# Optimization experiments

Measured on AMD Instinct MI355X. Metric: run time of the kernel, lower is better.

Reference implementation:

```python
import jax, jax.numpy as jnp
import numpy as np

LOG_SIG_MIN, LOG_SIG_MAX = -20.0, 2.0
BN_EPS = 1e-5

def leaky_relu(x):
    return jnp.where(x >= 0, x, 0.01 * x)

def setup_inputs() -> dict:
    key = jax.random.key(0)
    ks = jax.random.split(key, 12)
    E, B, N, H, A = 8, 16384, 64, 512, 8  # encoders, batch, nagents, hidden, heads
    d = H // A
    f32 = jnp.float32
    inp = {}
    inp['states'] = jax.random.normal(ks[0], (E, B, N), dtype=f32)
    inp['pre_actions'] = jax.random.normal(ks[1], (B, H), dtype=f32)
    inp['W_enc'] = jax.random.normal(ks[2], (E, N, H), dtype=f32) / np.sqrt(N)
    inp['b_enc'] = jnp.zeros((E, H), dtype=f32)
    inp['W_pre'] = jax.random.normal(ks[3], (H, H), dtype=f32) / np.sqrt(H)
    inp['b_pre'] = jnp.zeros((H,), dtype=f32)
    inp['Wk'] = jax.random.normal(ks[4], (A, H, d), dtype=f32) / np.sqrt(H)
    inp['Wsel'] = jax.random.normal(ks[5], (A, H, d), dtype=f32) / np.sqrt(H)
    inp['Wv'] = jax.random.normal(ks[6], (A, H, d), dtype=f32) / np.sqrt(H)
    inp['bv'] = jnp.zeros((A, d), dtype=f32)
    inp['W_actor'] = jax.random.normal(ks[7], (H, H), dtype=f32) / np.sqrt(H)
    inp['b_actor'] = jnp.zeros((H,), dtype=f32)
    inp['W_mean'] = jax.random.normal(ks[8], (H, N), dtype=f32) / np.sqrt(H)
    inp['b_mean'] = jnp.zeros((N,), dtype=f32)
    inp['W_logstd'] = jax.random.normal(ks[9], (H, N), dtype=f32) / np.sqrt(H)
    inp['b_logstd'] = jnp.zeros((N,), dtype=f32)
    return inp

def reference(states, pre_actions, W_enc, b_enc, W_pre, b_pre, Wk, Wsel, Wv, bv,
              W_actor, b_actor, W_mean, b_mean, W_logstd, b_logstd):
    # states: [E, B, N]; per-encoder BatchNorm1d (training-mode batch stats, no affine)
    mu = states.mean(axis=1, keepdims=True)                      # [E,1,N]
    var = states.var(axis=1, keepdims=True)                      # biased var, as torch BN
    s_norm = (states - mu) * jax.lax.rsqrt(var + BN_EPS)
    # per-encoder Linear + LeakyReLU -> encodings [E, B, H]
    encs = leaky_relu(jnp.einsum('ebn,enh->ebh', s_norm, W_enc) + b_enc[:, None, :])
    # per-head keys/values over all encoders: [A, E, B, d]
    keys = jnp.einsum('ebh,ahd->aebd', encs, Wk)
    vals = leaky_relu(jnp.einsum('ebh,ahd->aebd', encs, Wv) + bv[:, None, None, :])
    # selector from encoded previous actions: [A, B, d]
    pre = leaky_relu(pre_actions @ W_pre + b_pre)                 # [B, H]
    sel = jnp.einsum('bh,ahd->abd', pre, Wsel)
    d = keys.shape[-1]
    logits = jnp.einsum('abd,aebd->abe', sel, keys)               # [A, B, E]
    w = jax.nn.softmax(logits / np.sqrt(d), axis=-1)
    attn = jnp.einsum('aebd,abe->abd', vals, w)                   # [A, B, d]
    B = attn.shape[1]
    actor_in = jnp.transpose(attn, (1, 0, 2)).reshape(B, -1)      # [B, A*d] head-concat
    x = jax.nn.relu(actor_in @ W_actor + b_actor)
    mean = x @ W_mean + b_mean
    log_std = jnp.clip(x @ W_logstd + b_logstd, LOG_SIG_MIN, LOG_SIG_MAX)
    return mean, log_std, actor_in
```

## Files before the change

### kernel.cpp

```cpp
#include <hip/hip_runtime.h>
#include <hip/hip_bf16.h>
#include <stdint.h>

#define E_ 8
#define B_ 16384
#define N_ 64
#define H_ 512
#define A_ 8
#define D_ 64

typedef __hip_bfloat16 bf16;
typedef __attribute__((ext_vector_type(8))) short s8v;
typedef __attribute__((ext_vector_type(4))) float f4v;

__device__ __forceinline__ float bf2f(bf16 v) { return __bfloat162float(v); }
__device__ __forceinline__ bf16 f2bf(float v) { return __float2bfloat16(v); }
__device__ __forceinline__ short f2bfs(float v) {
    bf16 b = f2bf(v); short s; __builtin_memcpy(&s, &b, 2); return s;
}
__device__ __forceinline__ float bfs2f(short s) {
    bf16 b; __builtin_memcpy(&b, &s, 2); return bf2f(b);
}

__device__ __forceinline__ void async_load16(const void* g, void* l) {
    __builtin_amdgcn_global_load_lds(
        (const __attribute__((address_space(1))) void*)g,
        (__attribute__((address_space(3))) void*)l, 16, 0, 0);
}

__device__ __forceinline__ int swz_off(int row, int krow) {
    return row * 64 + (((krow >> 3) ^ (row & 7)) << 3);
}

template <int CB>
__device__ __forceinline__ void xcd_map(int x, int nBm, int& bm, int& bn) {
    if ((nBm & 7) == 0) {
        int j = x & 7, s = x >> 3;
        bn = s & ((1 << CB) - 1);
        bm = ((s >> CB) << 3) | j;
    } else {
        bm = x >> CB;
        bn = x & ((1 << CB) - 1);
    }
}

__global__ __launch_bounds__(256) void bnPart(const float* __restrict__ states,
                                              float* __restrict__ part,
                                              bf16* __restrict__ sbf) {
    int blk = blockIdx.x;
    int e = blk >> 6, sl = blk & 63;
    int tid = threadIdx.x, n = tid & 63, rg = tid >> 6;
    const long rowBase = (long)e * B_ + (long)sl * 256;
    const float* base = states + rowBase * 64;
    float s1 = 0.f, s2 = 0.f;
    for (int i = 0; i < 64; ++i) {
        float v = base[(rg + i * 4) * 64 + n];
        s1 += v; s2 += v * v;
        sbf[(rowBase + rg + i * 4) * 64 + n] = f2bf(v);
    }
    __shared__ float sh[2][4][64];
    sh[0][rg][n] = s1; sh[1][rg][n] = s2;
    __syncthreads();
    if (tid < 64) {
        float t1 = sh[0][0][n] + sh[0][1][n] + sh[0][2][n] + sh[0][3][n];
        float t2 = sh[1][0][n] + sh[1][1][n] + sh[1][2][n] + sh[1][3][n];
        part[((long)blk * 64 + n) * 2 + 0] = t1;
        part[((long)blk * 64 + n) * 2 + 1] = t2;
    }
}

__global__ void bnFin(const float* __restrict__ part, float* __restrict__ mu_rstd) {
    int idx = blockIdx.x * blockDim.x + threadIdx.x;
    if (idx >= E_ * 64) return;
    int e = idx >> 6, n = idx & 63;
    float s1 = 0.f, s2 = 0.f;
    for (int sl = 0; sl < 64; ++sl) {
        s1 += part[(((long)e * 64 + sl) * 64 + n) * 2 + 0];
        s2 += part[(((long)e * 64 + sl) * 64 + n) * 2 + 1];
    }
    float mu = s1 / (float)B_;
    float var = s2 / (float)B_ - mu * mu;
    mu_rstd[idx * 2 + 0] = mu;
    mu_rstd[idx * 2 + 1] = rsqrtf(var + 1e-5f);
}

__global__ void foldEnc(const float* __restrict__ W_enc, const float* __restrict__ b_enc,
                        const float* __restrict__ mu_rstd,
                        bf16* __restrict__ WencfT, float* __restrict__ bencf) {
    int idx = blockIdx.x * 256 + threadIdx.x;
    int e = idx >> 9, h = idx & 511;
    float acc = b_enc[e * 512 + h];
    for (int n = 0; n < 64; ++n) {
        float mu = mu_rstd[(e * 64 + n) * 2 + 0];
        float rs = mu_rstd[(e * 64 + n) * 2 + 1];
        float w = W_enc[((long)e * 64 + n) * 512 + h];
        WencfT[((long)e * 512 + h) * 64 + n] = f2bf(w * rs);
        acc -= mu * rs * w;
    }
    bencf[e * 512 + h] = acc;
}

__global__ __launch_bounds__(256) void packAll(
    const float* __restrict__ W_pre, const float* __restrict__ W_actor,
    const float* __restrict__ Wsel, const float* __restrict__ Wk,
    const float* __restrict__ Wv, const float* __restrict__ wm,
    const float* __restrict__ wl, const float* __restrict__ pre_actions,
    bf16* __restrict__ WpreT, bf16* __restrict__ WactorT, bf16* __restrict__ WselT,
    bf16* __restrict__ WkvaT, bf16* __restrict__ WmlT, bf16* __restrict__ pa_bf) {
    int bx = blockIdx.x, tid = threadIdx.x;
    if (bx < 2048) {
        const float* in = (bx < 1024) ? W_pre : W_actor;
        bf16* out = (bx < 1024) ? WpreT : WactorT;
        int idx = (bx & 1023) * 256 + tid;
        int n = idx >> 9, k = idx & 511;
        out[idx] = f2bf(in[k * 512 + n]);
    } else if (bx < 3072) {
        int idx = (bx - 2048) * 256 + tid;
        int n = idx >> 9, h = idx & 511;
        int a = n >> 6, dd = n & 63;
        WselT[idx] = f2bf(Wsel[((long)a * 512 + h) * 64 + dd]);
    } else if (bx < 5120) {
        int idx = (bx - 3072) * 256 + tid;
        int n = idx >> 9, h = idx & 511;
        int a = n >> 7, j = n & 127;
        const float* src = (j < 64) ? Wk : Wv;
        WkvaT[idx] = f2bf(src[((long)a * 512 + h) * 64 + (j & 63)]);
    } else if (bx < 5376) {
        int idx = (bx - 5120) * 256 + tid;
        int n = idx >> 9, k = idx & 511;
        float v = (n < 64) ? wm[k * 64 + n] : wl[k * 64 + (n - 64)];
        WmlT[idx] = f2bf(v);
    } else {
        int i = (bx - 5376) * 256 + tid;
        float4 v = ((const float4*)pre_actions)[i];
        bf16 o[4] = {f2bf(v.x), f2bf(v.y), f2bf(v.z), f2bf(v.w)};
        __builtin_memcpy(pa_bf + (long)i * 4, o, 8);
    }
}

template <int ACT, int OUTF, bool HAS_BIAS, int CB>
__global__ __launch_bounds__(256) void gemm_bt(
    const bf16* __restrict__ Ag, const bf16* __restrict__ Bg,
    const float* __restrict__ bias, const float* __restrict__ bias2,
    void* __restrict__ out, void* __restrict__ out2,
    int M, int Nn, int K, long sA, long sB, long sBias, long sO) {
    const int tid = threadIdx.x, lane = tid & 63, wid = tid >> 6;
    const int wm = wid >> 1, wn = wid & 1;
    int bm, bn;
    xcd_map<CB>(blockIdx.x, gridDim.x >> CB, bm, bn);
    const int bz = blockIdx.z;
    const bf16* Aptr = Ag + (long)bz * sA + (long)bm * 128 * K;
    const bf16* Bptr = Bg + (long)bz * sB + (long)bn * 128 * K;

    __shared__ __align__(16) short sAl[128 * 64];
    __shared__ __align__(16) short sBl[128 * 64];

    const int srow = lane >> 3;
    const int scol = (((lane & 7) ^ srow) << 3);

    f4v acc[4][4];
#pragma unroll
    for (int i = 0; i < 4; ++i)
#pragma unroll
        for (int j = 0; j < 4; ++j) acc[i][j] = f4v{0.f, 0.f, 0.f, 0.f};

    for (int k0 = 0; k0 < K; k0 += 64) {
#pragma unroll
        for (int i = 0; i < 4; ++i) {
            int r = (wid * 4 + i) * 8 + srow;
            async_load16(Aptr + (long)r * K + k0 + scol, (char*)sAl + (wid * 4 + i) * 1024);
            async_load16(Bptr + (long)r * K + k0 + scol, (char*)sBl + (wid * 4 + i) * 1024);
        }
        __syncthreads();
#pragma unroll
        for (int kk = 0; kk < 64; kk += 32) {
            int krow = kk + (lane >> 4) * 8;
            s8v af[4], bfr[4];
#pragma unroll
            for (int mi = 0; mi < 4; ++mi)
                af[mi] = *(const s8v*)(sAl + swz_off(wm * 64 + mi * 16 + (lane & 15), krow));
#pragma unroll
            for (int ni = 0; ni < 4; ++ni)
                bfr[ni] = *(const s8v*)(sBl + swz_off(wn * 64 + ni * 16 + (lane & 15), krow));
#pragma unroll
            for (int mi = 0; mi < 4; ++mi)
#pragma unroll
                for (int ni = 0; ni < 4; ++ni)
                    acc[mi][ni] = __builtin_amdgcn_mfma_f32_16x16x32_bf16(
                        af[mi], bfr[ni], acc[mi][ni], 0, 0, 0);
        }
        __syncthreads();
    }

    long m0 = (long)bm * 128 + wm * 64;
    long n0 = (long)bn * 128 + wn * 64;
#pragma unroll
    for (int mi = 0; mi < 4; ++mi)
#pragma unroll
        for (int ni = 0; ni < 4; ++ni)
#pragma unroll
            for (int r = 0; r < 4; ++r) {
                long gm = m0 + mi * 16 + (lane >> 4) * 4 + r;
                long gn = n0 + ni * 16 + (lane & 15);
                float v = acc[mi][ni][r];
                if constexpr (HAS_BIAS) v += bias[sBias * bz + gn];
                if constexpr (ACT == 1) v = (v >= 0.f) ? v : 0.01f * v;
                if constexpr (ACT == 2) v = fmaxf(v, 0.f);
                if constexpr (OUTF == 0) {
                    ((bf16*)out)[(long)bz * sO + gm * Nn + gn] = f2bf(v);
                } else if constexpr (OUTF == 1) {
                    ((float*)out)[(long)bz * sO + gm * Nn + gn] = v;
                } else if constexpr (OUTF == 2) {
                    if (gn < 64) {
                        ((float*)out)[gm * 64 + gn] = v + bias[gn];
                    } else {
                        float w = v + bias2[gn - 64];
                        w = fminf(fmaxf(w, -20.f), 2.f);
                        ((float*)out2)[gm * 64 + (gn - 64)] = w;
                    }
                } else {
                    ((bf16*)out)[(gm * E_ + bz) * 512 + gn] = f2bf(v);
                }
            }
}

__global__ __launch_bounds__(256) void kv_attn(
    const bf16* __restrict__ Ag, const bf16* __restrict__ Bg,
    const float* __restrict__ bv, const float* __restrict__ sel,
    float* __restrict__ actor_f32, bf16* __restrict__ attn_bf, int b0) {
    const int tid = threadIdx.x, lane = tid & 63, wid = tid >> 6;
    const int wm = wid >> 1, wn = wid & 1;
    int bm, a;
    xcd_map<3>(blockIdx.x, gridDim.x >> 3, bm, a);
    const bf16* Aptr = Ag + (long)bm * 128 * 512;
    const bf16* Bptr = Bg + (long)a * 128 * 512;

    __shared__ __align__(16) short sA[2 * 8192];
    __shared__ __align__(16) short sB[8192];
    __shared__ float lgs[128];

    const long bgBase = (long)b0 + (long)bm * 16;

    s8v bselH[2], bselL[2];
#pragma unroll
    for (int kk = 0; kk < 2; ++kk) {
        const float* sp = sel + (bgBase + (lane & 15)) * 512 + a * 64 + kk * 32 + (lane >> 4) * 8;
#pragma unroll
        for (int j = 0; j < 8; ++j) {
            float s = sp[j] * 0.125f;
            short h = f2bfs(s);
            bselH[kk][j] = h;
            bselL[kk][j] = f2bfs(s - bfs2f(h));
        }
    }

    const int srow = lane >> 3;
    const int scol = (((lane & 7) ^ srow) << 3);

    auto stageA = [&](int kt, int buf) {
#pragma unroll
        for (int i = 0; i < 4; ++i) {
            int r = (wid * 4 + i) * 8 + srow;
            async_load16(Aptr + (long)r * 512 + kt * 64 + scol,
                         (char*)(sA + buf * 8192) + (wid * 4 + i) * 1024);
        }
    };
    auto stageB = [&](int kt) {
#pragma unroll
        for (int i = 0; i < 4; ++i) {
            int r = (wid * 4 + i) * 8 + srow;
            async_load16(Bptr + (long)r * 512 + kt * 64 + scol,
                         (char*)sB + (wid * 4 + i) * 1024);
        }
    };

    f4v acc[4][4];
#pragma unroll
    for (int i = 0; i < 4; ++i)
#pragma unroll
        for (int j = 0; j < 4; ++j) acc[i][j] = f4v{0.f, 0.f, 0.f, 0.f};

    stageA(0, 0);
    stageB(0);
    __syncthreads();
    int cur = 0;
    for (int t = 0; t < 8; ++t) {
        if (t < 7) stageA(t + 1, cur ^ 1);
        const short* sAc = sA + cur * 8192;
#pragma unroll
        for (int kk = 0; kk < 64; kk += 32) {
            int krow = kk + (lane >> 4) * 8;
            s8v af[4], bfr[4];
#pragma unroll
            for (int mi = 0; mi < 4; ++mi)
                af[mi] = *(const s8v*)(sAc + swz_off(wm * 64 + mi * 16 + (lane & 15), krow));
#pragma unroll
            for (int ni = 0; ni < 4; ++ni)
                bfr[ni] = *(const s8v*)(sB + swz_off(wn * 64 + ni * 16 + (lane & 15), krow));
#pragma unroll
            for (int mi = 0; mi < 4; ++mi)
#pragma unroll
                for (int ni = 0; ni < 4; ++ni)
                    acc[mi][ni] = __builtin_amdgcn_mfma_f32_16x16x32_bf16(
                        af[mi], bfr[ni], acc[mi][ni], 0, 0, 0);
        }
        __syncthreads();
        if (t < 7) {
            stageB(t + 1);
            __syncthreads();
        }
        cur ^= 1;
    }

    short* keysC = sA;
    short* vT    = sB;
    const int quad = lane >> 4, cl = lane & 15;
#pragma unroll
    for (int mi = 0; mi < 4; ++mi)
#pragma unroll
        for (int ni = 0; ni < 4; ++ni)
#pragma unroll
            for (int r = 0; r < 4; ++r) {
                int row = wm * 64 + mi * 16 + quad * 4 + r;
                float v = acc[mi][ni][r];
                if (wn == 0) {
                    keysC[row * 72 + ni * 16 + cl] = f2bfs(v);
                } else {
                    int d = ni * 16 + cl;
                    v += bv[a * 64 + d];
                    v = (v >= 0.f) ? v : 0.01f * v;
                    vT[d * 128 + (row ^ ((d & 15) << 3))] = f2bfs(v);
                }
            }
    __syncthreads();

    {
        f4v lgacc[2] = {f4v{0.f, 0.f, 0.f, 0.f}, f4v{0.f, 0.f, 0.f, 0.f}};
#pragma unroll
        for (int kk = 0; kk < 2; ++kk) {
#pragma unroll
            for (int mi = 0; mi < 2; ++mi) {
                s8v af = *(const s8v*)(keysC + (wid * 32 + mi * 16 + cl) * 72 +
                                       kk * 32 + quad * 8);
                lgacc[mi] = __builtin_amdgcn_mfma_f32_16x16x32_bf16(
                    af, bselH[kk], lgacc[mi], 0, 0, 0);
                lgacc[mi] = __builtin_amdgcn_mfma_f32_16x16x32_bf16(
                    af, bselL[kk], lgacc[mi], 0, 0, 0);
            }
        }
#pragma unroll
        for (int mi = 0; mi < 2; ++mi)
#pragma unroll
            for (int r = 0; r < 4; ++r) {
                int grow = wid * 32 + mi * 16 + quad * 4 + r;
                if (cl == (grow >> 3)) lgs[grow] = lgacc[mi][r];
            }
    }
    __syncthreads();

#pragma unroll
    for (int t = 0; t < 4; ++t) {
        int lb = wid * 4 + t, row0 = lb * 8;
        s8v vvv = *(const s8v*)(vT + lane * 128 + (row0 ^ ((lane & 15) << 3)));
        float lg[8], vv[8];
#pragma unroll
        for (int e = 0; e < 8; ++e) {
            vv[e] = bfs2f(vvv[e]);
            lg[e] = lgs[row0 + e];
        }
        float mx = lg[0];
#pragma unroll
        for (int e = 1; e < 8; ++e) mx = fmaxf(mx, lg[e]);
        float ssum = 0.f, w[8];
#pragma unroll
        for (int e = 0; e < 8; ++e) { w[e] = __expf(lg[e] - mx); ssum += w[e]; }
        float inv = 1.f / ssum;
        float at = 0.f;
#pragma unroll
        for (int e = 0; e < 8; ++e) at += vv[e] * (w[e] * inv);
        long o = (bgBase + lb) * 512 + a * 64 + lane;
        actor_f32[o] = at;
        attn_bf[o] = f2bf(at);
    }
}

extern "C" void kernel_launch(void* const* d_in, const int* in_sizes, int n_in,
                              void* d_out, int out_size, void* d_ws, size_t ws_size,
                              hipStream_t stream) {
    (void)in_sizes; (void)n_in; (void)out_size;
    const float* states      = (const float*)d_in[0];
    const float* pre_actions = (const float*)d_in[1];
    const float* W_enc       = (const float*)d_in[2];
    const float* b_enc       = (const float*)d_in[3];
    const float* W_pre       = (const float*)d_in[4];
    const float* b_pre       = (const float*)d_in[5];
    const float* Wk          = (const float*)d_in[6];
    const float* Wsel        = (const float*)d_in[7];
    const float* Wv          = (const float*)d_in[8];
    const float* bv          = (const float*)d_in[9];
    const float* W_actor     = (const float*)d_in[10];
    const float* b_actor     = (const float*)d_in[11];
    const float* W_mean      = (const float*)d_in[12];
    const float* b_mean      = (const float*)d_in[13];
    const float* W_logstd    = (const float*)d_in[14];
    const float* b_logstd    = (const float*)d_in[15];

    char* ws = (char*)d_ws;
    size_t off = 0;
    auto alloc = [&](size_t bytes) -> void* {
        void* p = ws + off;
        off = (off + bytes + 255) & ~(size_t)255;
        return p;
    };
    float* mu_rstd = (float*)alloc((size_t)E_ * 64 * 2 * 4);
    float* bnpart  = (float*)alloc((size_t)E_ * 64 * 64 * 2 * 4);
    bf16* WencfT   = (bf16*)alloc((size_t)E_ * 512 * 64 * 2);
    float* bencf   = (float*)alloc((size_t)E_ * 512 * 4);
    bf16* WpreT    = (bf16*)alloc((size_t)512 * 512 * 2);
    bf16* WselT    = (bf16*)alloc((size_t)512 * 512 * 2);
    bf16* WkvaT    = (bf16*)alloc((size_t)1024 * 512 * 2);
    bf16* WactorT  = (bf16*)alloc((size_t)512 * 512 * 2);
    bf16* WmlT     = (bf16*)alloc((size_t)128 * 512 * 2);
    bf16* pa_bf    = (bf16*)alloc((size_t)B_ * 512 * 2);
    bf16* p_pre    = (bf16*)alloc((size_t)B_ * 512 * 2);
    float* p_sel   = (float*)alloc((size_t)B_ * 512 * 4);
    bf16* s_bf     = (bf16*)alloc((size_t)E_ * B_ * 64 * 2);
    bf16* p_attn = pa_bf;
    bf16* p_x    = p_pre;

    size_t remaining = (ws_size > off) ? ws_size - off : 0;
    int Bc = B_;
    while (Bc > 128 && (size_t)Bc * 8192 + 4096 > remaining) Bc >>= 1;
    const int NC = B_ / Bc;
    bf16* c_encs = (bf16*)alloc((size_t)E_ * Bc * 512 * 2);

    packAll<<<13568, 256, 0, stream>>>(W_pre, W_actor, Wsel, Wk, Wv, W_mean, W_logstd,
                                       pre_actions, WpreT, WactorT, WselT, WkvaT, WmlT,
                                       pa_bf);
    bnPart<<<512, 256, 0, stream>>>(states, bnpart, s_bf);
    bnFin<<<2, 256, 0, stream>>>(bnpart, mu_rstd);
    foldEnc<<<16, 256, 0, stream>>>(W_enc, b_enc, mu_rstd, WencfT, bencf);

    gemm_bt<1, 0, true, 2><<<dim3((B_ / 128) << 2, 1, 1), 256, 0, stream>>>(
        pa_bf, WpreT, b_pre, nullptr, p_pre, nullptr, B_, 512, 512, 0, 0, 0, 0);
    gemm_bt<0, 1, false, 2><<<dim3((B_ / 128) << 2, 1, 1), 256, 0, stream>>>(
        p_pre, WselT, nullptr, nullptr, p_sel, nullptr, B_, 512, 512, 0, 0, 0, 0);

    float* actor_out = (float*)d_out + 2L * B_ * 64;
    for (int c = 0; c < NC; ++c) {
        int b0 = c * Bc;
        gemm_bt<1, 4, true, 2><<<dim3((Bc / 128) << 2, 1, E_), 256, 0, stream>>>(
            s_bf + (long)b0 * 64, WencfT, bencf, nullptr, c_encs, nullptr, Bc, 512, 64,
            (long)B_ * 64, (long)512 * 64, 512, 0);
        kv_attn<<<dim3((Bc / 16) * 8, 1, 1), 256, 0, stream>>>(
            c_encs, WkvaT, bv, p_sel, actor_out, p_attn, b0);
    }

    gemm_bt<2, 0, true, 2><<<dim3((B_ / 128) << 2, 1, 1), 256, 0, stream>>>(
        p_attn, WactorT, b_actor, nullptr, p_x, nullptr, B_, 512, 512, 0, 0, 0, 0);
    gemm_bt<0, 2, false, 0><<<dim3(B_ / 128, 1, 1), 256, 0, stream>>>(
        p_x, WmlT, b_mean, b_logstd, (float*)d_out, (float*)d_out + (long)B_ * 64,
        B_, 128, 512, 0, 0, 0, 0);
}
```

Baseline: 556.7 us.

## Process two attention heads per kv_attn block to reuse encoder tiles

Each kv_attn block now computes keys and values for two heads, using a 128x256 output tile instead of 128x128, so every staged encoder (A) tile is reused across twice as many MFMA columns and the grid is halved. Shared memory grows to 64 KB plus logits, the per-thread accumulator array doubles to 32 f4v, and the keys buffer moves to a swizzled 64-wide layout. This cuts redundant global reads of the encodings but raises register and LDS pressure, which can lower occupancy.

```diff
diff --git a/kernel.cpp b/kernel.cpp
--- a/kernel.cpp
+++ b/kernel.cpp
@@ -230,21 +230,22 @@
     float* __restrict__ actor_f32, bf16* __restrict__ attn_bf, int b0) {
     const int tid = threadIdx.x, lane = tid & 63, wid = tid >> 6;
     const int wm = wid >> 1, wn = wid & 1;
-    int bm, a;
-    xcd_map<3>(blockIdx.x, gridDim.x >> 3, bm, a);
+    int bm, hp;
+    xcd_map<2>(blockIdx.x, gridDim.x >> 2, bm, hp);
     const bf16* Aptr = Ag + (long)bm * 128 * 512;
-    const bf16* Bptr = Bg + (long)a * 128 * 512;
-
-    __shared__ __align__(16) short sA[2 * 8192];
-    __shared__ __align__(16) short sB[8192];
-    __shared__ float lgs[128];
+    const bf16* Bptr = Bg + (long)hp * 256 * 512;
+
+    __shared__ __align__(16) short smem[32768];
+    __shared__ float lgs[2][128];
 
     const long bgBase = (long)b0 + (long)bm * 16;
+    const int myh = wid & 1;
 
     s8v bselH[2], bselL[2];
 #pragma unroll
     for (int kk = 0; kk < 2; ++kk) {
-        const float* sp = sel + (bgBase + (lane & 15)) * 512 + a * 64 + kk * 32 + (lane >> 4) * 8;
+        const float* sp = sel + (bgBase + (lane & 15)) * 512 + (hp * 2 + myh) * 64 +
+                          kk * 32 + (lane >> 4) * 8;
 #pragma unroll
         for (int j = 0; j < 8; ++j) {
             float s = sp[j] * 0.125f;
@@ -262,23 +263,23 @@
         for (int i = 0; i < 4; ++i) {
             int r = (wid * 4 + i) * 8 + srow;
             async_load16(Aptr + (long)r * 512 + kt * 64 + scol,
-                         (char*)(sA + buf * 8192) + (wid * 4 + i) * 1024);
+                         (char*)(smem + buf * 8192) + (wid * 4 + i) * 1024);
         }
     };
     auto stageB = [&](int kt) {
 #pragma unroll
-        for (int i = 0; i < 4; ++i) {
-            int r = (wid * 4 + i) * 8 + srow;
+        for (int i = 0; i < 8; ++i) {
+            int r = (wid * 8 + i) * 8 + srow;
             async_load16(Bptr + (long)r * 512 + kt * 64 + scol,
-                         (char*)sB + (wid * 4 + i) * 1024);
+                         (char*)(smem + 16384) + (wid * 8 + i) * 1024);
         }
     };
 
-    f4v acc[4][4];
+    f4v acc[4][8];
 #pragma unroll
     for (int i = 0; i < 4; ++i)
 #pragma unroll
-        for (int j = 0; j < 4; ++j) acc[i][j] = f4v{0.f, 0.f, 0.f, 0.f};
+        for (int j = 0; j < 8; ++j) acc[i][j] = f4v{0.f, 0.f, 0.f, 0.f};
 
     stageA(0, 0);
     stageB(0);
@@ -286,21 +287,22 @@
     int cur = 0;
     for (int t = 0; t < 8; ++t) {
         if (t < 7) stageA(t + 1, cur ^ 1);
-        const short* sAc = sA + cur * 8192;
+        const short* sAc = smem + cur * 8192;
+        const short* sBc = smem + 16384;
 #pragma unroll
         for (int kk = 0; kk < 64; kk += 32) {
             int krow = kk + (lane >> 4) * 8;
-            s8v af[4], bfr[4];
+            s8v af[4], bfr[8];
 #pragma unroll
             for (int mi = 0; mi < 4; ++mi)
                 af[mi] = *(const s8v*)(sAc + swz_off(wm * 64 + mi * 16 + (lane & 15), krow));
 #pragma unroll
-            for (int ni = 0; ni < 4; ++ni)
-                bfr[ni] = *(const s8v*)(sB + swz_off(wn * 64 + ni * 16 + (lane & 15), krow));
+            for (int ni = 0; ni < 8; ++ni)
+                bfr[ni] = *(const s8v*)(sBc + swz_off(wn * 128 + ni * 16 + (lane & 15), krow));
 #pragma unroll
             for (int mi = 0; mi < 4; ++mi)
 #pragma unroll
-                for (int ni = 0; ni < 4; ++ni)
+                for (int ni = 0; ni < 8; ++ni)
                     acc[mi][ni] = __builtin_amdgcn_mfma_f32_16x16x32_bf16(
                         af[mi], bfr[ni], acc[mi][ni], 0, 0, 0);
         }
@@ -312,61 +314,66 @@
         cur ^= 1;
     }
 
-    short* keysC = sA;
-    short* vT    = sB;
     const int quad = lane >> 4, cl = lane & 15;
-#pragma unroll
-    for (int mi = 0; mi < 4; ++mi)
-#pragma unroll
-        for (int ni = 0; ni < 4; ++ni)
-#pragma unroll
-            for (int r = 0; r < 4; ++r) {
-                int row = wm * 64 + mi * 16 + quad * 4 + r;
-                float v = acc[mi][ni][r];
-                if (wn == 0) {
-                    keysC[row * 72 + ni * 16 + cl] = f2bfs(v);
-                } else {
-                    int d = ni * 16 + cl;
-                    v += bv[a * 64 + d];
-                    v = (v >= 0.f) ? v : 0.01f * v;
-                    vT[d * 128 + (row ^ ((d & 15) << 3))] = f2bfs(v);
+    {
+        short* keysC_h = smem + wn * 8192;
+        short* vT_h    = smem + 16384 + wn * 8192;
+#pragma unroll
+        for (int mi = 0; mi < 4; ++mi)
+#pragma unroll
+            for (int ni = 0; ni < 8; ++ni)
+#pragma unroll
+                for (int r = 0; r < 4; ++r) {
+                    int row = wm * 64 + mi * 16 + quad * 4 + r;
+                    float v = acc[mi][ni][r];
+                    if (ni < 4) {
+                        int g = ni * 2 + (cl >> 3);
+                        keysC_h[row * 64 + (((g ^ (row & 7)) << 3) | (cl & 7))] = f2bfs(v);
+                    } else {
+                        int d = (ni - 4) * 16 + cl;
+                        v += bv[(hp * 2 + wn) * 64 + d];
+                        v = (v >= 0.f) ? v : 0.01f * v;
+                        vT_h[d * 128 + (row ^ ((d & 15) << 3))] = f2bfs(v);
+                    }
                 }
-            }
+    }
     __syncthreads();
 
     {
-        f4v lgacc[2] = {f4v{0.f, 0.f, 0.f, 0.f}, f4v{0.f, 0.f, 0.f, 0.f}};
-#pragma unroll
-        for (int kk = 0; kk < 2; ++kk) {
-#pragma unroll
-            for (int mi = 0; mi < 2; ++mi) {
-                s8v af = *(const s8v*)(keysC + (wid * 32 + mi * 16 + cl) * 72 +
-                                       kk * 32 + quad * 8);
+        const short* kc = smem + myh * 8192;
+        const int rb = (wid >> 1) * 64;
+        f4v lgacc[4] = {f4v{0.f, 0.f, 0.f, 0.f}, f4v{0.f, 0.f, 0.f, 0.f},
+                        f4v{0.f, 0.f, 0.f, 0.f}, f4v{0.f, 0.f, 0.f, 0.f}};
+#pragma unroll
+        for (int kk = 0; kk < 2; ++kk)
+#pragma unroll
+            for (int mi = 0; mi < 4; ++mi) {
+                s8v af = *(const s8v*)(kc + swz_off(rb + mi * 16 + cl, kk * 32 + quad * 8));
                 lgacc[mi] = __builtin_amdgcn_mfma_f32_16x16x32_bf16(
                     af, bselH[kk], lgacc[mi], 0, 0, 0);
                 lgacc[mi] = __builtin_amdgcn_mfma_f32_16x16x32_bf16(
                     af, bselL[kk], lgacc[mi], 0, 0, 0);
             }
-        }
-#pragma unroll
-        for (int mi = 0; mi < 2; ++mi)
+#pragma unroll
+        for (int mi = 0; mi < 4; ++mi)
 #pragma unroll
             for (int r = 0; r < 4; ++r) {
-                int grow = wid * 32 + mi * 16 + quad * 4 + r;
-                if (cl == (grow >> 3)) lgs[grow] = lgacc[mi][r];
+                int grow = rb + mi * 16 + quad * 4 + r;
+                if (cl == (grow >> 3)) lgs[myh][grow] = lgacc[mi][r];
             }
     }
     __syncthreads();
 
-#pragma unroll
-    for (int t = 0; t < 4; ++t) {
-        int lb = wid * 4 + t, row0 = lb * 8;
-        s8v vvv = *(const s8v*)(vT + lane * 128 + (row0 ^ ((lane & 15) << 3)));
+    const short* vp = smem + 16384 + myh * 8192;
+#pragma unroll
+    for (int t = 0; t < 8; ++t) {
+        int lb = (wid >> 1) * 8 + t, row0 = lb * 8;
+        s8v vvv = *(const s8v*)(vp + lane * 128 + (row0 ^ ((lane & 15) << 3)));
         float lg[8], vv[8];
 #pragma unroll
         for (int e = 0; e < 8; ++e) {
             vv[e] = bfs2f(vvv[e]);
-            lg[e] = lgs[row0 + e];
+            lg[e] = lgs[myh][row0 + e];
         }
         float mx = lg[0];
 #pragma unroll
@@ -378,7 +385,7 @@
         float at = 0.f;
 #pragma unroll
         for (int e = 0; e < 8; ++e) at += vv[e] * (w[e] * inv);
-        long o = (bgBase + lb) * 512 + a * 64 + lane;
+        long o = (bgBase + lb) * 512 + (hp * 2 + myh) * 64 + lane;
         actor_f32[o] = at;
         attn_bf[o] = f2bf(at);
     }
@@ -452,7 +459,7 @@
         gemm_bt<1, 4, true, 2><<<dim3((Bc / 128) << 2, 1, E_), 256, 0, stream>>>(
             s_bf + (long)b0 * 64, WencfT, bencf, nullptr, c_encs, nullptr, Bc, 512, 64,
             (long)B_ * 64, (long)512 * 64, 512, 0);
-        kv_attn<<<dim3((Bc / 16) * 8, 1, 1), 256, 0, stream>>>(
+        kv_attn<<<dim3((Bc / 16) * 4, 1, 1), 256, 0, stream>>>(
             c_encs, WkvaT, bv, p_sel, actor_out, p_attn, b0);
     }
 
```

Result: faster. 537.1 us (-3.5%).
